# Kernel optimization log

Measured on AMD Instinct MI355X. Metric: run time of the kernel, lower is better.

## Reference

```python
import jax, jax.numpy as jnp
import numpy as np

HID = 64   # hid_dim // 2 inside pocket_att_net2
H = 8      # n_heads


def _dist_mask(d):
    """get_mask: 8 distance bands, each carrying 1/d inside its band, else 0.
    band i (i=0..6): i < d <= i+3 ; band 7: d > 7.  Output [B, 8, Nl, Np]."""
    safe = jnp.where(d > 0, d, 1.0)
    inv = jnp.where(d > 0, 1.0 / safe, 0.0)
    bands = []
    for i in range(8):
        if i < 7:
            m = (d > float(i)) & (d <= float(i + 3))
        else:
            m = d > 7.0
        bands.append(jnp.where(m, inv, 0.0))
    return jnp.stack(bands, axis=1)


def setup_inputs() -> dict:
    key = jax.random.key(0)
    ks = jax.random.split(key, 20)
    B, Nl, Np = 16, 256, 2048
    s = 0.05
    inp = {
        "ligand": jax.random.normal(ks[0], (B, Nl, HID), jnp.float32),
        "prot":   jax.random.normal(ks[1], (B, Np, HID), jnp.float32),
        "dist":   jax.random.uniform(ks[2], (B, Nl, Np), jnp.float32) * 10.0,
        # projection weights (jax convention: x @ W + b)
        "w_l1": jax.random.normal(ks[3], (HID, HID * H), jnp.float32) * s,
        "b_l1": jnp.zeros((HID * H,), jnp.float32),
        "w_l2": jax.random.normal(ks[4], (HID, HID * H), jnp.float32) * s,
        "b_l2": jnp.zeros((HID * H,), jnp.float32),
        "w_p1": jax.random.normal(ks[5], (HID, HID * H), jnp.float32) * s,
        "b_p1": jnp.zeros((HID * H,), jnp.float32),
        "w_p2": jax.random.normal(ks[6], (HID, HID * H), jnp.float32) * s,
        "b_p2": jnp.zeros((HID * H,), jnp.float32),
        "fc11_w": jax.random.normal(ks[7], (HID * H, HID), jnp.float32) * s,
        "fc11_b": jnp.zeros((HID,), jnp.float32),
        "fc12_w": jax.random.normal(ks[8], (2 * HID, HID), jnp.float32) * s,
        "fc12_b": jnp.zeros((HID,), jnp.float32),
        "fc21_w": jax.random.normal(ks[9], (HID * H, HID), jnp.float32) * s,
        "fc21_b": jnp.zeros((HID,), jnp.float32),
        "fc22_w": jax.random.normal(ks[10], (2 * HID, HID), jnp.float32) * s,
        "fc22_b": jnp.zeros((HID,), jnp.float32),
    }
    return inp


def _proj(x, w, b):
    B, N, _ = x.shape
    h = jax.nn.relu(x @ w + b)                      # [B, N, H*HID]
    return h.reshape(B, N, H, HID).transpose(0, 2, 1, 3)  # [B, H, N, HID]


def reference(ligand, prot, dist, w_l1, b_l1, w_l2, b_l2, w_p1, b_p1, w_p2, b_p2,
              fc11_w, fc11_b, fc12_w, fc12_b, fc21_w, fc21_b, fc22_w, fc22_b):
    B, Nl, _ = ligand.shape
    Np = prot.shape[1]
    inter = _dist_mask(dist)                        # [B, H, Nl, Np]

    l1 = _proj(ligand, w_l1, b_l1)
    l2 = _proj(ligand, w_l2, b_l2)
    p1 = _proj(prot, w_p1, b_p1)
    p2 = _proj(prot, w_p2, b_p2)

    scale = jnp.sqrt(jnp.float32(HID))
    energy = jnp.einsum('bhld,bhpd->bhlp', l1, p1) / scale
    att = jax.nn.softmax(energy * inter, axis=-1)   # dropout = identity (eval)

    l3 = jnp.einsum('bhlp,bhpd->bhld', att, p2)
    l3 = l3.transpose(0, 2, 1, 3).reshape(B, Nl, H * HID)
    l3 = jnp.concatenate([l3 @ fc11_w + fc11_b, ligand], axis=2)
    l3 = jax.nn.relu(l3 @ fc12_w + fc12_b)          # [B, Nl, HID]

    p3 = jnp.einsum('bhlp,bhld->bhpd', att, l2)
    p3 = p3.transpose(0, 2, 1, 3).reshape(B, Np, H * HID)
    p3 = jnp.concatenate([p3 @ fc21_w + fc21_b, prot], axis=2)
    p3 = jax.nn.relu(p3 @ fc22_w + fc22_b)          # [B, Np, HID]

    return jnp.concatenate([l3, p3], axis=1)        # [B, Nl+Np, HID]
```

## Files before the change

kernel.cpp:

```cpp
#include <hip/hip_runtime.h>
#include <hip/hip_bf16.h>

typedef _Float16 f16x8 __attribute__((ext_vector_type(8)));
typedef _Float16 f16x4 __attribute__((ext_vector_type(4)));
typedef float f32x4 __attribute__((ext_vector_type(4)));

#define B_   16
#define NL   256
#define NP   2048
#define NH   8
#define PSPLIT 4
#define PCHUNK (NP / PSPLIT)

static __device__ __forceinline__ f32x4 mfma16(f16x8 a, f16x8 b, f32x4 c) {
  return __builtin_amdgcn_mfma_f32_16x16x32_f16(a, b, c, 0, 0, 0);
}

__global__ __launch_bounds__(256) void proj_kernel(
    const float* __restrict__ x, const float* __restrict__ W, const float* __restrict__ bias,
    _Float16* __restrict__ outA, _Float16* __restrict__ outB, int N, int mode)
{
  __shared__ float xt[64][68];
  const int t = threadIdx.x;
  const int n0 = blockIdx.x * 64;
  const int h  = blockIdx.y;
  const int b  = blockIdx.z;

  const float* xp = x + ((size_t)b * N + n0) * 64;
#pragma unroll
  for (int i = 0; i < 4; ++i) {
    int flat = (i * 256 + t) * 4;
    f32x4 v = *(const f32x4*)(xp + flat);
    *(f32x4*)&xt[flat >> 6][flat & 63] = v;
  }
  __syncthreads();

  const int nb = (t >> 4) * 4;
  const int db = (t & 15) * 4;

  float acc[4][4];
#pragma unroll
  for (int i = 0; i < 4; ++i)
#pragma unroll
    for (int j = 0; j < 4; ++j) acc[i][j] = bias[h * 64 + db + j];

  const float* wp = W + h * 64 + db;
#pragma unroll 8
  for (int k = 0; k < 64; ++k) {
    f32x4 wq = *(const f32x4*)(wp + (size_t)k * 512);
    float a0 = xt[nb + 0][k], a1 = xt[nb + 1][k], a2 = xt[nb + 2][k], a3 = xt[nb + 3][k];
#pragma unroll
    for (int j = 0; j < 4; ++j) {
      acc[0][j] += a0 * wq[j];
      acc[1][j] += a1 * wq[j];
      acc[2][j] += a2 * wq[j];
      acc[3][j] += a3 * wq[j];
    }
  }

  if (mode == 0) {
#pragma unroll
    for (int i = 0; i < 4; ++i) {
      f16x4 hv, lv;
#pragma unroll
      for (int j = 0; j < 4; ++j) {
        float v = fmaxf(acc[i][j], 0.f);
        _Float16 hi = (_Float16)v;
        hv[j] = hi;
        lv[j] = (_Float16)((v - (float)hi) * 2048.0f);
      }
      size_t idx = (((size_t)b * NH + h) * N + n0 + nb + i) * 64 + db;
      *(f16x4*)(outA + idx) = hv;
      *(f16x4*)(outB + idx) = lv;
    }
  } else {
#pragma unroll
    for (int j = 0; j < 4; ++j) {
      f16x4 tv;
#pragma unroll
      for (int i = 0; i < 4; ++i) tv[i] = (_Float16)fmaxf(acc[i][j], 0.f);
      size_t idx = (((size_t)b * NH + h) * 64 + db + j) * N + n0 + nb;
      *(f16x4*)(outA + idx) = tv;
    }
  }
}

__global__ __launch_bounds__(512) void flash_l3_kernel(
    const _Float16* __restrict__ l1h, const _Float16* __restrict__ l1l,
    const _Float16* __restrict__ p1h, const _Float16* __restrict__ p1l,
    const _Float16* __restrict__ p2t, const float* __restrict__ dist,
    float* __restrict__ l3p, float* __restrict__ mpart, float* __restrict__ spart)
{
  const int lt = blockIdx.x;
  const int sp = blockIdx.y;
  const int b  = blockIdx.z;
  const int t  = threadIdx.x;
  const int h    = t >> 6;
  const int lane = t & 63;
  const int g = lane >> 4, c = lane & 15;
  const int l0 = lt * 16;
  const int bh = b * NH + h;

  __shared__ float distT[64][20];
  __shared__ _Float16 P[NH][16][72];

  const size_t l1off = ((size_t)bh * NL + l0 + c) * 64;
  f16x8 aLh[2], aLl[2];
  aLh[0] = *(const f16x8*)(l1h + l1off + g * 8);
  aLh[1] = *(const f16x8*)(l1h + l1off + 32 + g * 8);
  aLl[0] = *(const f16x8*)(l1l + l1off + g * 8);
  aLl[1] = *(const f16x8*)(l1l + l1off + 32 + g * 8);

  f32x4 accO[4];
#pragma unroll
  for (int dt = 0; dt < 4; ++dt) accO[dt] = (f32x4){0.f, 0.f, 0.f, 0.f};
  float m_r[4] = {-INFINITY, -INFINITY, -INFINITY, -INFINITY};
  float s_r[4] = {0.f, 0.f, 0.f, 0.f};

  const float* dbase = dist + ((size_t)b * NL + l0) * NP + sp * PCHUNK;
  const _Float16* p1hb = p1h + ((size_t)bh * NP + sp * PCHUNK) * 64;
  const _Float16* p1lb = p1l + ((size_t)bh * NP + sp * PCHUNK) * 64;
  const _Float16* p2tb = p2t + (size_t)bh * 64 * NP + sp * PCHUNK;
  const float fh = (float)h, fh3 = fh + 3.0f;

  const int dl_p = t & 63;
  const int dl_l = t >> 6;

  for (int P0 = 0; P0 < PCHUNK; P0 += 64) {
    float dv0 = dbase[(size_t)dl_l * NP + P0 + dl_p];
    float dv1 = dbase[(size_t)(dl_l + 8) * NP + P0 + dl_p];
    __syncthreads();
    distT[dl_p][dl_l]     = dv0;
    distT[dl_p][dl_l + 8] = dv1;
    __syncthreads();

    float mev[4][4];
    float cmax[4] = {-INFINITY, -INFINITY, -INFINITY, -INFINITY};
#pragma unroll
    for (int s = 0; s < 4; ++s) {
      const _Float16* ph = p1hb + (size_t)(P0 + s * 16 + c) * 64;
      const _Float16* pl = p1lb + (size_t)(P0 + s * 16 + c) * 64;
      f16x8 bh0 = *(const f16x8*)(ph + g * 8);
      f16x8 bh1 = *(const f16x8*)(ph + 32 + g * 8);
      f16x8 bl0 = *(const f16x8*)(pl + g * 8);
      f16x8 bl1 = *(const f16x8*)(pl + 32 + g * 8);
      f32x4 e  = (f32x4){0.f, 0.f, 0.f, 0.f};
      f32x4 ec = (f32x4){0.f, 0.f, 0.f, 0.f};
      e  = mfma16(aLh[0], bh0, e);  e  = mfma16(aLh[1], bh1, e);
      ec = mfma16(aLh[0], bl0, ec); ec = mfma16(aLh[1], bl1, ec);
      ec = mfma16(aLl[0], bh0, ec); ec = mfma16(aLl[1], bh1, ec);
      f32x4 dq = *(const f32x4*)&distT[s * 16 + c][g * 4];
#pragma unroll
      for (int r = 0; r < 4; ++r) {
        float dv = dq[r];
        float ev = (e[r] + ec[r] * (1.0f / 2048.0f)) * 0.125f;
        bool cond = (h < 7) ? (dv > fh && dv <= fh3) : (dv > 7.0f);
        float m = cond ? ev * __builtin_amdgcn_rcpf(dv) : 0.0f;
        mev[s][r] = m;
        cmax[r] = fmaxf(cmax[r], m);
      }
    }
#pragma unroll
    for (int mask = 1; mask < 16; mask <<= 1)
#pragma unroll
      for (int r = 0; r < 4; ++r)
        cmax[r] = fmaxf(cmax[r], __shfl_xor(cmax[r], mask, 64));

#pragma unroll
    for (int r = 0; r < 4; ++r) {
      float mn  = fmaxf(m_r[r], cmax[r]);
      float fac = __expf(m_r[r] - mn);
      m_r[r] = mn;
      float ss = 0.f;
#pragma unroll
      for (int s = 0; s < 4; ++s) {
        float pv = __expf(mev[s][r] - mn);
        ss += pv;
        P[h][g * 4 + r][s * 16 + c] = (_Float16)pv;
      }
      s_r[r] = s_r[r] * fac + ss;
#pragma unroll
      for (int dt = 0; dt < 4; ++dt) accO[dt][r] *= fac;
    }
    __syncthreads();
#pragma unroll
    for (int kk = 0; kk < 2; ++kk) {
      f16x8 aP = *(const f16x8*)&P[h][c][kk * 32 + g * 8];
#pragma unroll
      for (int dt = 0; dt < 4; ++dt) {
        f16x8 bV = *(const f16x8*)(p2tb + (size_t)(dt * 16 + c) * NP + P0 + kk * 32 + g * 8);
        accO[dt] = mfma16(aP, bV, accO[dt]);
      }
    }
  }

#pragma unroll
  for (int mask = 1; mask < 16; mask <<= 1)
#pragma unroll
    for (int r = 0; r < 4; ++r) s_r[r] += __shfl_xor(s_r[r], mask, 64);

  float* lp = l3p + (size_t)sp * B_ * NL * 512;
#pragma unroll
  for (int dt = 0; dt < 4; ++dt)
#pragma unroll
    for (int r = 0; r < 4; ++r)
      lp[((size_t)b * NL + l0 + g * 4 + r) * 512 + h * 64 + dt * 16 + c] = accO[dt][r];

  if (c == 0) {
#pragma unroll
    for (int r = 0; r < 4; ++r) {
      size_t li = (size_t)sp * B_ * NH * NL + (size_t)bh * NL + l0 + g * 4 + r;
      mpart[li] = m_r[r];
      spart[li] = s_r[r];
    }
  }
}

__global__ __launch_bounds__(256) void merge_l3_kernel(
    const float* __restrict__ l3p, const float* __restrict__ mpart, const float* __restrict__ spart,
    float* __restrict__ l3c, float* __restrict__ mrow, float* __restrict__ rsrow)
{
  const int row = blockIdx.x * 4 + (threadIdx.x >> 6);
  const int d   = threadIdx.x & 63;
  const int l   = row & (NL - 1);
  const int bh  = row >> 8;
  const int b = bh >> 3, h = bh & 7;
  const size_t srow = (size_t)B_ * NH * NL;

  float mi[PSPLIT], si[PSPLIT];
  float M = -INFINITY;
#pragma unroll
  for (int i = 0; i < PSPLIT; ++i) {
    mi[i] = mpart[(size_t)i * srow + row];
    si[i] = spart[(size_t)i * srow + row];
    M = fmaxf(M, mi[i]);
  }
  const float* lp = l3p + ((size_t)b * NL + l) * 512 + h * 64 + d;
  float S = 0.f, o = 0.f;
#pragma unroll
  for (int i = 0; i < PSPLIT; ++i) {
    float w = __expf(mi[i] - M);
    S += si[i] * w;
    o += lp[(size_t)i * B_ * NL * 512] * w;
  }
  float rs = 1.0f / S;
  l3c[((size_t)b * NL + l) * 512 + h * 64 + d] = o * rs;
  if (d == 0) { mrow[row] = M; rsrow[row] = rs; }
}

__global__ __launch_bounds__(512) void p3_kernel(
    const _Float16* __restrict__ p1h, const _Float16* __restrict__ p1l,
    const _Float16* __restrict__ l1h, const _Float16* __restrict__ l1l,
    const _Float16* __restrict__ l2t, const float* __restrict__ dist,
    const float* __restrict__ mrow, const float* __restrict__ rsrow,
    float* __restrict__ p3c)
{
  const int pt = blockIdx.x;
  const int b  = blockIdx.y;
  const int t  = threadIdx.x;
  const int h    = t >> 6;
  const int lane = t & 63;
  const int g = lane >> 4, c = lane & 15;
  const int p0 = pt * 16;
  const int bh = b * NH + h;

  __shared__ float distT[32][20];
  __shared__ _Float16 PT[NH][16][40];

  const size_t poff = ((size_t)bh * NP + p0 + c) * 64;
  f16x8 aPh[2], aPl[2];
  aPh[0] = *(const f16x8*)(p1h + poff + g * 8);
  aPh[1] = *(const f16x8*)(p1h + poff + 32 + g * 8);
  aPl[0] = *(const f16x8*)(p1l + poff + g * 8);
  aPl[1] = *(const f16x8*)(p1l + poff + 32 + g * 8);

  f32x4 acc[4];
#pragma unroll
  for (int dt = 0; dt < 4; ++dt) acc[dt] = (f32x4){0.f, 0.f, 0.f, 0.f};

  const float* db_ = dist + (size_t)b * NL * NP + p0;
  const _Float16* l1hb = l1h + (size_t)bh * NL * 64;
  const _Float16* l1lb = l1l + (size_t)bh * NL * 64;
  const _Float16* l2tb = l2t + (size_t)bh * 64 * NL;
  const float* mb = mrow + (size_t)bh * NL;
  const float* rb = rsrow + (size_t)bh * NL;
  const float fh = (float)h, fh3 = fh + 3.0f;

  const int dl_l = t >> 4;
  const int dl_p = t & 15;

  for (int lc = 0; lc < NL; lc += 32) {
    float dv = db_[(size_t)(lc + dl_l) * NP + dl_p];
    __syncthreads();
    distT[dl_l][dl_p] = dv;
    __syncthreads();

#pragma unroll
    for (int s = 0; s < 2; ++s) {
      const int l = lc + s * 16 + c;
      const _Float16* lhp = l1hb + (size_t)l * 64;
      const _Float16* llp = l1lb + (size_t)l * 64;
      f16x8 bh0 = *(const f16x8*)(lhp + g * 8);
      f16x8 bh1 = *(const f16x8*)(lhp + 32 + g * 8);
      f16x8 bl0 = *(const f16x8*)(llp + g * 8);
      f16x8 bl1 = *(const f16x8*)(llp + 32 + g * 8);
      f32x4 e  = (f32x4){0.f, 0.f, 0.f, 0.f};
      f32x4 ec = (f32x4){0.f, 0.f, 0.f, 0.f};
      e  = mfma16(aPh[0], bh0, e);  e  = mfma16(aPh[1], bh1, e);
      ec = mfma16(aPh[0], bl0, ec); ec = mfma16(aPh[1], bl1, ec);
      ec = mfma16(aPl[0], bh0, ec); ec = mfma16(aPl[1], bh1, ec);
      float ml = mb[l], rl = rb[l];
      f32x4 dq = *(const f32x4*)&distT[s * 16 + c][g * 4];
#pragma unroll
      for (int r = 0; r < 4; ++r) {
        float ev = (e[r] + ec[r] * (1.0f / 2048.0f)) * 0.125f;
        float dvv = dq[r];
        bool cond = (h < 7) ? (dvv > fh && dvv <= fh3) : (dvv > 7.0f);
        float m = cond ? ev * __builtin_amdgcn_rcpf(dvv) : 0.0f;
        float att = __expf(m - ml) * rl;
        PT[h][g * 4 + r][s * 16 + c] = (_Float16)att;
      }
    }
    __syncthreads();
    {
      f16x8 aA = *(const f16x8*)&PT[h][c][g * 8];
#pragma unroll
      for (int dt = 0; dt < 4; ++dt) {
        f16x8 bV = *(const f16x8*)(l2tb + (size_t)(dt * 16 + c) * NL + lc + g * 8);
        acc[dt] = mfma16(aA, bV, acc[dt]);
      }
    }
  }

#pragma unroll
  for (int dt = 0; dt < 4; ++dt)
#pragma unroll
    for (int r = 0; r < 4; ++r)
      p3c[((size_t)b * NP + p0 + g * 4 + r) * 512 + h * 64 + dt * 16 + c] = acc[dt][r];
}

__global__ __launch_bounds__(256) void fc_out_kernel(
    const float* __restrict__ x3c, const float* __restrict__ xbase,
    const float* __restrict__ wA, const float* __restrict__ bA,
    const float* __restrict__ wB, const float* __restrict__ bB,
    float* __restrict__ out, int N, int out_off)
{
  __shared__ float xl[16][520];
  __shared__ float t1[16][68];
  __shared__ float xb[16][68];
  const int t = threadIdx.x;
  const int row0 = blockIdx.x * 16;

  const float* xp = x3c + (size_t)row0 * 512;
#pragma unroll
  for (int i = 0; i < 8; ++i) {
    int flat = (i * 256 + t) * 4;
    f32x4 v = *(const f32x4*)(xp + flat);
    *(f32x4*)&xl[flat >> 9][flat & 511] = v;
  }
  {
    const float* bp = xbase + (size_t)row0 * 64;
    int flat = t * 4;
    f32x4 v = *(const f32x4*)(bp + flat);
    *(f32x4*)&xb[flat >> 6][flat & 63] = v;
  }
  __syncthreads();

  const int r  = t >> 4;
  const int c4 = (t & 15) * 4;

  float acc[4];
#pragma unroll
  for (int j = 0; j < 4; ++j) acc[j] = bA[c4 + j];
  for (int k4 = 0; k4 < 128; ++k4) {
    f32x4 xq = *(const f32x4*)&xl[r][k4 * 4];
#pragma unroll
    for (int kk = 0; kk < 4; ++kk) {
      f32x4 wq = *(const f32x4*)(wA + (size_t)(k4 * 4 + kk) * 64 + c4);
#pragma unroll
      for (int j = 0; j < 4; ++j) acc[j] += xq[kk] * wq[j];
    }
  }
#pragma unroll
  for (int j = 0; j < 4; ++j) t1[r][c4 + j] = acc[j];
  __syncthreads();

  float a2[4];
#pragma unroll
  for (int j = 0; j < 4; ++j) a2[j] = bB[c4 + j];
  for (int k4 = 0; k4 < 32; ++k4) {
    f32x4 xq = (k4 < 16) ? *(const f32x4*)&t1[r][k4 * 4]
                         : *(const f32x4*)&xb[r][k4 * 4 - 64];
#pragma unroll
    for (int kk = 0; kk < 4; ++kk) {
      f32x4 wq = *(const f32x4*)(wB + (size_t)(k4 * 4 + kk) * 64 + c4);
#pragma unroll
      for (int j = 0; j < 4; ++j) a2[j] += xq[kk] * wq[j];
    }
  }
  const int row = row0 + r;
  const int b = row / N, n = row % N;
  f32x4 o;
#pragma unroll
  for (int j = 0; j < 4; ++j) o[j] = fmaxf(a2[j], 0.f);
  *(f32x4*)(out + (((size_t)b * (NL + NP)) + out_off + n) * 64 + c4) = o;
}

extern "C" void kernel_launch(void* const* d_in, const int* in_sizes, int n_in,
                              void* d_out, int out_size, void* d_ws, size_t ws_size,
                              hipStream_t stream)
{
  const float* ligand = (const float*)d_in[0];
  const float* prot   = (const float*)d_in[1];
  const float* dist   = (const float*)d_in[2];
  const float* w_l1   = (const float*)d_in[3];
  const float* b_l1   = (const float*)d_in[4];
  const float* w_l2   = (const float*)d_in[5];
  const float* b_l2   = (const float*)d_in[6];
  const float* w_p1   = (const float*)d_in[7];
  const float* b_p1   = (const float*)d_in[8];
  const float* w_p2   = (const float*)d_in[9];
  const float* b_p2   = (const float*)d_in[10];
  const float* fc11_w = (const float*)d_in[11];
  const float* fc11_b = (const float*)d_in[12];
  const float* fc12_w = (const float*)d_in[13];
  const float* fc12_b = (const float*)d_in[14];
  const float* fc21_w = (const float*)d_in[15];
  const float* fc21_b = (const float*)d_in[16];
  const float* fc22_w = (const float*)d_in[17];
  const float* fc22_b = (const float*)d_in[18];
  float* out = (float*)d_out;

  char* ws = (char*)d_ws;
  size_t off = 0;
  auto alloc = [&](size_t bytes) -> void* {
    void* p = ws + off;
    off += (bytes + 255) & ~(size_t)255;
    return p;
  };
  const size_t L1E = (size_t)B_ * NH * NL * 64;
  const size_t P1E = (size_t)B_ * NH * NP * 64;
  _Float16* l1h = (_Float16*)alloc(L1E * 2);
  _Float16* l1l = (_Float16*)alloc(L1E * 2);
  _Float16* p1h = (_Float16*)alloc(P1E * 2);
  _Float16* p1l = (_Float16*)alloc(P1E * 2);
  _Float16* l2t = (_Float16*)alloc(L1E * 2);
  _Float16* p2t = (_Float16*)alloc(P1E * 2);
  float* mrow  = (float*)alloc((size_t)B_ * NH * NL * 4);
  float* rsrow = (float*)alloc((size_t)B_ * NH * NL * 4);
  float* mpart = (float*)alloc((size_t)PSPLIT * B_ * NH * NL * 4);
  float* spart = (float*)alloc((size_t)PSPLIT * B_ * NH * NL * 4);
  float* l3c = (float*)alloc((size_t)B_ * NL * 512 * 4);
  float* p3c = (float*)alloc((size_t)B_ * NP * 512 * 4);
  float* l3p = p3c;

  proj_kernel<<<dim3(NL / 64, NH, B_), 256, 0, stream>>>(ligand, w_l1, b_l1, l1h, l1l, NL, 0);
  proj_kernel<<<dim3(NL / 64, NH, B_), 256, 0, stream>>>(ligand, w_l2, b_l2, l2t, nullptr, NL, 1);
  proj_kernel<<<dim3(NP / 64, NH, B_), 256, 0, stream>>>(prot, w_p1, b_p1, p1h, p1l, NP, 0);
  proj_kernel<<<dim3(NP / 64, NH, B_), 256, 0, stream>>>(prot, w_p2, b_p2, p2t, nullptr, NP, 1);

  flash_l3_kernel<<<dim3(NL / 16, PSPLIT, B_), 512, 0, stream>>>(
      l1h, l1l, p1h, p1l, p2t, dist, l3p, mpart, spart);
  merge_l3_kernel<<<(B_ * NH * NL) / 4, 256, 0, stream>>>(l3p, mpart, spart, l3c, mrow, rsrow);
  p3_kernel<<<dim3(NP / 16, B_), 512, 0, stream>>>(p1h, p1l, l1h, l1l, l2t, dist,
                                                   mrow, rsrow, p3c);

  fc_out_kernel<<<(B_ * NL) / 16, 256, 0, stream>>>(l3c, ligand, fc11_w, fc11_b,
                                                    fc12_w, fc12_b, out, NL, 0);
  fc_out_kernel<<<(B_ * NP) / 16, 256, 0, stream>>>(p3c, prot, fc21_w, fc21_b,
                                                    fc22_w, fc22_b, out, NP, NL);
}
```

Baseline: 799.5 us.

## Load distances directly from global memory and reorder attention kernel grids

Both attention kernels stop staging the distance tile through shared memory. Each lane now reads its own distance values straight from global memory, which also removes two block-wide barriers per iteration plus the barrier before the per-wave P tile is read. The grid dimensions are also permuted so that batch and split indices vary fastest, changing which blocks run concurrently and how they share cache. The cost is that all eight head-waves now fetch the same distance data separately, leaning on L1/L2 hits, and the flash kernel does narrower strided loads.

```diff
diff --git a/kernel.cpp b/kernel.cpp
--- a/kernel.cpp
+++ b/kernel.cpp
@@ -91,9 +91,10 @@
     const _Float16* __restrict__ p2t, const float* __restrict__ dist,
     float* __restrict__ l3p, float* __restrict__ mpart, float* __restrict__ spart)
 {
-  const int lt = blockIdx.x;
-  const int sp = blockIdx.y;
-  const int b  = blockIdx.z;
+  const int sb = blockIdx.x;
+  const int sp = sb & (PSPLIT - 1);
+  const int b  = sb >> 2;
+  const int lt = blockIdx.y;
   const int t  = threadIdx.x;
   const int h    = t >> 6;
   const int lane = t & 63;
@@ -101,7 +102,6 @@
   const int l0 = lt * 16;
   const int bh = b * NH + h;
 
-  __shared__ float distT[64][20];
   __shared__ _Float16 P[NH][16][72];
 
   const size_t l1off = ((size_t)bh * NL + l0 + c) * 64;
@@ -123,17 +123,7 @@
   const _Float16* p2tb = p2t + (size_t)bh * 64 * NP + sp * PCHUNK;
   const float fh = (float)h, fh3 = fh + 3.0f;
 
-  const int dl_p = t & 63;
-  const int dl_l = t >> 6;
-
   for (int P0 = 0; P0 < PCHUNK; P0 += 64) {
-    float dv0 = dbase[(size_t)dl_l * NP + P0 + dl_p];
-    float dv1 = dbase[(size_t)(dl_l + 8) * NP + P0 + dl_p];
-    __syncthreads();
-    distT[dl_p][dl_l]     = dv0;
-    distT[dl_p][dl_l + 8] = dv1;
-    __syncthreads();
-
     float mev[4][4];
     float cmax[4] = {-INFINITY, -INFINITY, -INFINITY, -INFINITY};
 #pragma unroll
@@ -144,12 +134,17 @@
       f16x8 bh1 = *(const f16x8*)(ph + 32 + g * 8);
       f16x8 bl0 = *(const f16x8*)(pl + g * 8);
       f16x8 bl1 = *(const f16x8*)(pl + 32 + g * 8);
+      const float* drow = dbase + P0 + s * 16 + c;
+      float d0 = drow[(size_t)(g * 4 + 0) * NP];
+      float d1 = drow[(size_t)(g * 4 + 1) * NP];
+      float d2 = drow[(size_t)(g * 4 + 2) * NP];
+      float d3 = drow[(size_t)(g * 4 + 3) * NP];
       f32x4 e  = (f32x4){0.f, 0.f, 0.f, 0.f};
       f32x4 ec = (f32x4){0.f, 0.f, 0.f, 0.f};
       e  = mfma16(aLh[0], bh0, e);  e  = mfma16(aLh[1], bh1, e);
       ec = mfma16(aLh[0], bl0, ec); ec = mfma16(aLh[1], bl1, ec);
       ec = mfma16(aLl[0], bh0, ec); ec = mfma16(aLl[1], bh1, ec);
-      f32x4 dq = *(const f32x4*)&distT[s * 16 + c][g * 4];
+      f32x4 dq = (f32x4){d0, d1, d2, d3};
 #pragma unroll
       for (int r = 0; r < 4; ++r) {
         float dv = dq[r];
@@ -182,7 +177,6 @@
 #pragma unroll
       for (int dt = 0; dt < 4; ++dt) accO[dt][r] *= fac;
     }
-    __syncthreads();
 #pragma unroll
     for (int kk = 0; kk < 2; ++kk) {
       f16x8 aP = *(const f16x8*)&P[h][c][kk * 32 + g * 8];
@@ -255,8 +249,8 @@
     const float* __restrict__ mrow, const float* __restrict__ rsrow,
     float* __restrict__ p3c)
 {
-  const int pt = blockIdx.x;
-  const int b  = blockIdx.y;
+  const int b  = blockIdx.x;
+  const int pt = blockIdx.y;
   const int t  = threadIdx.x;
   const int h    = t >> 6;
   const int lane = t & 63;
@@ -264,7 +258,6 @@
   const int p0 = pt * 16;
   const int bh = b * NH + h;
 
-  __shared__ float distT[32][20];
   __shared__ _Float16 PT[NH][16][40];
 
   const size_t poff = ((size_t)bh * NP + p0 + c) * 64;
@@ -286,15 +279,7 @@
   const float* rb = rsrow + (size_t)bh * NL;
   const float fh = (float)h, fh3 = fh + 3.0f;
 
-  const int dl_l = t >> 4;
-  const int dl_p = t & 15;
-
   for (int lc = 0; lc < NL; lc += 32) {
-    float dv = db_[(size_t)(lc + dl_l) * NP + dl_p];
-    __syncthreads();
-    distT[dl_l][dl_p] = dv;
-    __syncthreads();
-
 #pragma unroll
     for (int s = 0; s < 2; ++s) {
       const int l = lc + s * 16 + c;
@@ -310,7 +295,7 @@
       ec = mfma16(aPh[0], bl0, ec); ec = mfma16(aPh[1], bl1, ec);
       ec = mfma16(aPl[0], bh0, ec); ec = mfma16(aPl[1], bh1, ec);
       float ml = mb[l], rl = rb[l];
-      f32x4 dq = *(const f32x4*)&distT[s * 16 + c][g * 4];
+      f32x4 dq = *(const f32x4*)(db_ + (size_t)l * NP + g * 4);
 #pragma unroll
       for (int r = 0; r < 4; ++r) {
         float ev = (e[r] + ec[r] * (1.0f / 2048.0f)) * 0.125f;
@@ -321,7 +306,6 @@
         PT[h][g * 4 + r][s * 16 + c] = (_Float16)att;
       }
     }
-    __syncthreads();
     {
       f16x8 aA = *(const f16x8*)&PT[h][c][g * 8];
 #pragma unroll
@@ -459,10 +443,10 @@
   proj_kernel<<<dim3(NP / 64, NH, B_), 256, 0, stream>>>(prot, w_p1, b_p1, p1h, p1l, NP, 0);
   proj_kernel<<<dim3(NP / 64, NH, B_), 256, 0, stream>>>(prot, w_p2, b_p2, p2t, nullptr, NP, 1);
 
-  flash_l3_kernel<<<dim3(NL / 16, PSPLIT, B_), 512, 0, stream>>>(
+  flash_l3_kernel<<<dim3(PSPLIT * B_, NL / 16), 512, 0, stream>>>(
       l1h, l1l, p1h, p1l, p2t, dist, l3p, mpart, spart);
   merge_l3_kernel<<<(B_ * NH * NL) / 4, 256, 0, stream>>>(l3p, mpart, spart, l3c, mrow, rsrow);
-  p3_kernel<<<dim3(NP / 16, B_), 512, 0, stream>>>(p1h, p1l, l1h, l1l, l2t, dist,
+  p3_kernel<<<dim3(B_, NP / 16), 512, 0, stream>>>(p1h, p1l, l1h, l1l, l2t, dist,
                                                    mrow, rsrow, p3c);
 
   fc_out_kernel<<<(B_ * NL) / 16, 256, 0, stream>>>(l3c, ligand, fc11_w, fc11_b,
```

New measurement: 840.4 us. +5.1%, slower.
